# Optimization experiments

Measured on AMD Instinct MI355X. Metric: run time of the kernel, lower is better.

Reference implementation:

```python
import jax, jax.numpy as jnp
import numpy as np

H, W = 64, 64

def _fft_mask(h, w):
    # matches torch: W -> W//2+1 for rfft; linspace(-1,1,H) x linspace(0,1,W//2+1)
    wr = w // 2 + 1
    ys = np.linspace(-1.0, 1.0, h)
    xs = np.linspace(0.0, 1.0, wr)
    Y, X = np.meshgrid(ys, xs, indexing='ij')
    return (np.abs(X) < 0.1) | (np.abs(Y) < 0.1) | (X ** 2 + Y ** 2 <= 0.4 ** 2)

_MASK = _fft_mask(H, W)
_IY, _IX = np.nonzero(_MASK)            # static gather indices, K = mask.sum()
_K = int(_MASK.sum())


def setup_inputs() -> dict:
    key = jax.random.key(0)
    k1, k2, k3 = jax.random.split(key, 3)
    S, P, C = 16, 256, 3
    enc_dim = 1024
    mask_dim = 6 * _K                    # real+imag, C=3 channels -> 2*3*K
    x = jax.random.normal(k1, (S, P, C, H, W), dtype=jnp.float32)
    bc_mask = jnp.zeros((H, W), dtype=bool)
    proj_w = jax.random.normal(k2, (enc_dim, mask_dim), dtype=jnp.float32) / np.sqrt(mask_dim)
    proj_b = jax.random.normal(k3, (enc_dim,), dtype=jnp.float32) * 0.01
    return {"x": x, "bc_mask": bc_mask, "proj_w": proj_w, "proj_b": proj_b}


def reference(x, bc_mask, proj_w, proj_b):
    S, P, C = x.shape[0], x.shape[1], x.shape[2]
    fft_x = jnp.fft.rfft2(x)                       # (S,P,C,H,W//2+1) complex
    fft_x = jnp.fft.fftshift(fft_x, axes=-2)       # shift along H
    # boolean-mask gather (row-major over (H, W//2+1) per (s,p,c)), then flatten C*K
    filt = fft_x[..., _IY, _IX]                    # (S,P,C,K)
    filt = filt.reshape(S, P, C * _K)
    feats = jnp.concatenate([jnp.real(filt), jnp.imag(filt)], axis=-1)  # (S,P,6K)
    return feats @ proj_w.T + proj_b               # (S,P,enc_dim)
```

## Files before the change

### kernel.cpp

```cpp
#include <hip/hip_runtime.h>
#include <hip/hip_bf16.h>
#include <math.h>

typedef float f32x4 __attribute__((ext_vector_type(4)));
typedef __bf16 bf16x8 __attribute__((ext_vector_type(8)));

#define PI2 6.283185307179586

static __device__ __forceinline__ unsigned short f2b(float f) {
  __hip_bfloat16 h = __float2bfloat16(f);
  return reinterpret_cast<unsigned short&>(h);
}

__global__ __launch_bounds__(256) void setup_tables_kernel(
    unsigned short* __restrict__ post16, __hip_bfloat16* __restrict__ Tt,
    __hip_bfloat16* __restrict__ Ub) {
  const int tid = threadIdx.x;
  __shared__ int cnt[64];
  __shared__ int pref[64];

  if (tid < 64) {
    int i = tid;
    double ys = -1.0 + (double)i * (2.0 / 63.0);
    int cRow = 0;
    for (int j = 0; j < 33; ++j) {
      double xs = (double)j / 32.0;
      bool m = (fabs(xs) < 0.1) || (fabs(ys) < 0.1) || (xs * xs + ys * ys <= 0.16);
      cRow += m ? 1 : 0;
    }
    cnt[i] = cRow;
  }
  __syncthreads();
  if (tid == 0) {
    int s = 0;
    for (int i = 0; i < 64; ++i) { pref[i] = s; s += cnt[i]; }
  }
  __syncthreads();
  if (tid < 64) {
    int i = tid;
    int k = pref[i];
    double ys = -1.0 + (double)i * (2.0 / 63.0);
    for (int j = 0; j < 36; ++j) {
      unsigned short v = 0xFFFFu;
      if (j < 33) {
        double xs = (double)j / 32.0;
        bool m = (fabs(xs) < 0.1) || (fabs(ys) < 0.1) || (xs * xs + ys * ys <= 0.16);
        if (m) v = (unsigned short)(k++);
      }
      post16[i * 36 + j] = v;
    }
  }

  for (int idx = tid; idx < 80 * 64; idx += 256) {
    int n = idx >> 6, w = idx & 63;
    float v = 0.0f;
    if (n < 33) {
      int r = (n * w) & 63;
      v = cosf((float)(PI2 / 64.0) * (float)r);
    } else if (n >= 40 && n < 73) {
      int r = ((n - 40) * w) & 63;
      v = -sinf((float)(PI2 / 64.0) * (float)r);
    }
    Tt[idx] = __float2bfloat16(v);
  }

  for (int idx = tid; idx < 128 * 128; idx += 256) {
    int up = idx >> 7, kk = idx & 127;
    int u = up & 63;
    int vfreq = (u + 32) & 63;
    int h = kk & 63;
    int r = (vfreq * h) & 63;
    float cv, sv;
    __sincosf((float)(PI2 / 64.0) * (float)r, &sv, &cv);
    float val;
    if (up < 64) val = (kk < 64) ? cv : sv;
    else         val = (kk < 64) ? -sv : cv;
    Ub[idx] = __float2bfloat16(val);
  }
}

__global__ __launch_bounds__(256) void wconv_kernel(
    const float* __restrict__ W, __hip_bfloat16* __restrict__ wB,
    int N, int Kd, int Kp) {
  int total = N * Kp;
  for (int idx = blockIdx.x * 256 + threadIdx.x; idx < total; idx += gridDim.x * 256) {
    int e = idx / Kp;
    int f = idx - e * Kp;
    float v = (f < Kd) ? W[(size_t)e * Kd + f] : 0.0f;
    wB[idx] = __float2bfloat16(v);
  }
}

#define IMGB 10880
#define POSTB 4608

__global__ __launch_bounds__(256, 4) void fft_mfma_kernel(
    const float* __restrict__ x,
    const __hip_bfloat16* __restrict__ Tt,
    const __hip_bfloat16* __restrict__ Ub,
    const unsigned short* __restrict__ post16,
    __hip_bfloat16* __restrict__ feats,
    int K, int Kp) {
  __shared__ __align__(16) char lds[2 * IMGB + POSTB];
  const int tid = threadIdx.x;
  const int lane = tid & 63;
  const int w = tid >> 6;
  const int wi = w >> 1;
  const int wp = w & 1;
  const int l4 = lane & 15;
  const int q = lane >> 4;
  const int img = blockIdx.x * 2 + wi;
  const int sp = img / 3;
  const int c = img - sp * 3;
  char* ibuf = lds + wi * IMGB;
  unsigned int* fb = (unsigned int*)(ibuf + 8704);
  unsigned short* fbs = (unsigned short*)fb;
  unsigned short* postl = (unsigned short*)(lds + 2 * IMGB);

  const float* xi = x + (size_t)img * 4096;
  float4 st[8];
  #pragma unroll
  for (int r = 0; r < 8; ++r) {
    int row = wp * 32 + r * 4 + q;
    st[r] = *reinterpret_cast<const float4*>(xi + row * 64 + l4 * 4);
  }
  {
    const unsigned int* src = reinterpret_cast<const unsigned int*>(post16);
    unsigned int* dst = reinterpret_cast<unsigned int*>(postl);
    for (int i = tid; i < 1152; i += 256) dst[i] = src[i];
  }
  #pragma unroll
  for (int r = 0; r < 8; ++r) {
    int row = wp * 32 + r * 4 + q;
    int off = row * 128 + (((l4 >> 1) ^ (row & 7)) * 16 + (l4 & 1) * 8);
    ushort4 b;
    b.x = f2b(st[r].x); b.y = f2b(st[r].y); b.z = f2b(st[r].z); b.w = f2b(st[r].w);
    *reinterpret_cast<ushort4*>(ibuf + off) = b;
  }

  f32x4 acc1[2][5] = {};
  #pragma unroll
  for (int ks = 0; ks < 2; ++ks) {
    bf16x8 a1[2], b1[5];
    #pragma unroll
    for (int am = 0; am < 2; ++am) {
      int h = (wp * 2 + am) * 16 + l4;
      int kg = ks * 4 + q;
      a1[am] = *reinterpret_cast<const bf16x8*>(ibuf + h * 128 + ((kg ^ (h & 7)) * 16));
    }
    #pragma unroll
    for (int n = 0; n < 5; ++n) {
      int row = n * 16 + l4;
      b1[n] = *reinterpret_cast<const bf16x8*>(
          (const char*)Tt + row * 128 + ks * 64 + q * 16);
    }
    #pragma unroll
    for (int am = 0; am < 2; ++am)
      #pragma unroll
      for (int n = 0; n < 5; ++n)
        acc1[am][n] = __builtin_amdgcn_mfma_f32_16x16x32_bf16(a1[am], b1[n], acc1[am][n], 0, 0, 0);
  }

  __syncthreads();

  #pragma unroll
  for (int n = 0; n < 5; ++n) {
    int col = n * 16 + l4;
    bool isRe = (col < 33);
    bool isIm = (col >= 40 && col < 73);
    if (!(isRe || isIm)) continue;
    int j = isRe ? col : (col - 40);
    #pragma unroll
    for (int am = 0; am < 2; ++am) {
      #pragma unroll
      for (int r = 0; r < 4; ++r) {
        int h = (wp * 2 + am) * 16 + q * 4 + r;
        int kk = isRe ? h : (h + 64);
        int off = j * 256 + (((kk >> 3) ^ (j & 15)) * 16 + (kk & 7) * 2);
        *reinterpret_cast<unsigned short*>(ibuf + off) = f2b(acc1[am][n][r]);
      }
    }
  }

  __syncthreads();

  f32x4 acc2[3][4] = {};
  #pragma unroll
  for (int ks = 0; ks < 4; ++ks) {
    bf16x8 a2[3], b2[4];
    #pragma unroll
    for (int m = 0; m < 3; ++m) {
      int j = m * 16 + l4;
      if (j > 33) j = 33;
      int kg = ks * 4 + q;
      a2[m] = *reinterpret_cast<const bf16x8*>(ibuf + j * 256 + ((kg ^ (j & 15)) * 16));
    }
    #pragma unroll
    for (int n = 0; n < 4; ++n) {
      int rowg = (wp * 4 + n) * 16 + l4;
      b2[n] = *reinterpret_cast<const bf16x8*>(
          (const char*)Ub + rowg * 256 + ks * 64 + q * 16);
    }
    #pragma unroll
    for (int m = 0; m < 3; ++m)
      #pragma unroll
      for (int n = 0; n < 4; ++n)
        acc2[m][n] = __builtin_amdgcn_mfma_f32_16x16x32_bf16(a2[m], b2[n], acc2[m][n], 0, 0, 0);
  }

  const int base = wp ? K : 0;
  #pragma unroll
  for (int n = 0; n < 4; ++n) {
    int u = n * 16 + l4;
    #pragma unroll
    for (int m = 0; m < 3; ++m) {
      int j0 = m * 16 + q * 4;
      if (j0 > 32) continue;
      ushort4 kv = *reinterpret_cast<const ushort4*>(postl + u * 36 + j0);
      #pragma unroll
      for (int r = 0; r < 4; ++r) {
        int j = j0 + r;
        unsigned short k = (&kv.x)[r];
        if (j < 33 && k != 0xFFFFu)
          fbs[base + k] = f2b(acc2[m][n][r]);
      }
    }
  }

  __syncthreads();

  {
    size_t obase = (size_t)sp * Kp;
    unsigned int* gRe = reinterpret_cast<unsigned int*>(feats + obase + (size_t)c * K);
    unsigned int* gIm = reinterpret_cast<unsigned int*>(feats + obase + (size_t)3 * K + (size_t)c * K);
    const int KD2 = K / 2;
    for (int i = wp * 64 + lane; i < KD2; i += 128) {
      gRe[i] = fb[i];
      gIm[i] = fb[KD2 + i];
    }
    if (wp == 0 && c == 2) {
      unsigned int* gp = reinterpret_cast<unsigned int*>(feats + obase + (size_t)6 * K);
      int padDw = (Kp - 6 * K) / 2;
      if (lane < padDw) gp[lane] = 0u;
    }
  }
}

#define BM 128
#define BN 128
#define BKK 64

__global__ __launch_bounds__(256) void gemm_bias_kernel(
    const __hip_bfloat16* __restrict__ A, const __hip_bfloat16* __restrict__ B,
    const float* __restrict__ bias, float* __restrict__ C,
    int M, int N, int Kp) {
  __shared__ __align__(16) unsigned short As[BM * BKK];
  __shared__ __align__(16) unsigned short Bs[BN * BKK];

  const int tid = threadIdx.x;
  const int lane = tid & 63;
  const int wid = tid >> 6;
  const int wm = wid & 1;
  const int wn = wid >> 1;
  const int nbm = M / BM;
  const int bm = blockIdx.x % nbm;
  const int bn = blockIdx.x / nbm;
  const int row0A = bm * BM;
  const int row0B = bn * BN;

  f32x4 acc[4][4] = {};

  for (int k0 = 0; k0 < Kp; k0 += BKK) {
    #pragma unroll
    for (int i = 0; i < 4; ++i) {
      int qc = i * 256 + tid;
      int r = qc >> 3;
      int cb = (qc & 7) * 16;
      const char* gA = (const char*)A + ((size_t)(row0A + r) * Kp + k0) * 2 + cb;
      const char* gB = (const char*)B + ((size_t)(row0B + r) * Kp + k0) * 2 + cb;
      char* lA = (char*)As + (size_t)(i * 256 + wid * 64) * 16;
      char* lB = (char*)Bs + (size_t)(i * 256 + wid * 64) * 16;
      __builtin_amdgcn_global_load_lds((const __attribute__((address_space(1))) void*)gA,
                                       (__attribute__((address_space(3))) void*)lA, 16, 0, 0);
      __builtin_amdgcn_global_load_lds((const __attribute__((address_space(1))) void*)gB,
                                       (__attribute__((address_space(3))) void*)lB, 16, 0, 0);
    }
    __syncthreads();

    #pragma unroll
    for (int kk = 0; kk < 2; ++kk) {
      bf16x8 afr[4], bfr[4];
      const int ke = kk * 32 + (lane >> 4) * 8;
      #pragma unroll
      for (int m = 0; m < 4; ++m) {
        int rowA = wm * 64 + m * 16 + (lane & 15);
        afr[m] = *reinterpret_cast<const bf16x8*>(&As[rowA * BKK + ke]);
      }
      #pragma unroll
      for (int n = 0; n < 4; ++n) {
        int rowB = wn * 64 + n * 16 + (lane & 15);
        bfr[n] = *reinterpret_cast<const bf16x8*>(&Bs[rowB * BKK + ke]);
      }
      #pragma unroll
      for (int m = 0; m < 4; ++m)
        #pragma unroll
        for (int n = 0; n < 4; ++n)
          acc[m][n] = __builtin_amdgcn_mfma_f32_16x16x32_bf16(afr[m], bfr[n], acc[m][n], 0, 0, 0);
    }
    __syncthreads();
  }

  #pragma unroll
  for (int n = 0; n < 4; ++n) {
    int gcol = row0B + wn * 64 + n * 16 + (lane & 15);
    float bv = bias[gcol];
    #pragma unroll
    for (int m = 0; m < 4; ++m) {
      int grow0 = row0A + wm * 64 + m * 16 + (lane >> 4) * 4;
      #pragma unroll
      for (int r = 0; r < 4; ++r) {
        C[(size_t)(grow0 + r) * N + gcol] = acc[m][n][r] + bv;
      }
    }
  }
}

extern "C" void kernel_launch(void* const* d_in, const int* in_sizes, int n_in,
                              void* d_out, int out_size, void* d_ws, size_t ws_size,
                              hipStream_t stream) {
  const float* x = (const float*)d_in[0];
  const float* W = (const float*)d_in[2];
  const float* bias = (const float*)d_in[3];
  float* out = (float*)d_out;

  const int ENC = in_sizes[3];
  const int Kd = in_sizes[2] / ENC;
  const int K = Kd / 6;
  const int NIMG = in_sizes[0] / 4096;
  const int SP = NIMG / 3;
  const int Kp = (Kd + 63) & ~63;

  char* ws = (char*)d_ws;
  unsigned short* post16 = (unsigned short*)ws;
  __hip_bfloat16* Tt = (__hip_bfloat16*)(ws + 9216);
  __hip_bfloat16* Ub = (__hip_bfloat16*)(ws + 19456);
  __hip_bfloat16* wB = (__hip_bfloat16*)(ws + 52224);
  size_t wBytes = (size_t)ENC * Kp * 2;
  __hip_bfloat16* feats = (__hip_bfloat16*)(ws + 52224 + wBytes);

  setup_tables_kernel<<<1, 256, 0, stream>>>(post16, Tt, Ub);
  wconv_kernel<<<1024, 256, 0, stream>>>(W, wB, ENC, Kd, Kp);
  fft_mfma_kernel<<<NIMG / 2, 256, 0, stream>>>(x, Tt, Ub, post16, feats, K, Kp);
  gemm_bias_kernel<<<(SP / BM) * (ENC / BN), 256, 0, stream>>>(feats, wB, bias, out, SP, ENC, Kp);
}
```

Before: 191.7 us.

## Loop FFT blocks over eight images with register prefetch of next image

Each FFT block now uses two waves instead of four and processes eight images in sequence rather than two in parallel. The post-index table is copied to LDS once per eight images instead of once per two. While the current image's second-stage MFMAs run, the next image's global loads are issued into registers. The stage-1 spectrum write-back now uses vectorized ushort4 stores. In exchange, far fewer waves are launched, so less parallelism is available to hide memory latency, and images within a block are processed serially.

```diff
diff --git a/kernel.cpp b/kernel.cpp
--- a/kernel.cpp
+++ b/kernel.cpp
@@ -91,157 +91,187 @@
   }
 }
 
+#define IMGS 8
 #define IMGB 10880
 #define POSTB 4608
 
-__global__ __launch_bounds__(256, 4) void fft_mfma_kernel(
+__global__ __launch_bounds__(128, 4) void fft_mfma_kernel(
     const float* __restrict__ x,
     const __hip_bfloat16* __restrict__ Tt,
     const __hip_bfloat16* __restrict__ Ub,
     const unsigned short* __restrict__ post16,
     __hip_bfloat16* __restrict__ feats,
     int K, int Kp) {
-  __shared__ __align__(16) char lds[2 * IMGB + POSTB];
+  __shared__ __align__(16) char lds[IMGB + POSTB];
   const int tid = threadIdx.x;
   const int lane = tid & 63;
-  const int w = tid >> 6;
-  const int wi = w >> 1;
-  const int wp = w & 1;
+  const int wp = tid >> 6;
   const int l4 = lane & 15;
   const int q = lane >> 4;
-  const int img = blockIdx.x * 2 + wi;
-  const int sp = img / 3;
-  const int c = img - sp * 3;
-  char* ibuf = lds + wi * IMGB;
-  unsigned int* fb = (unsigned int*)(ibuf + 8704);
+  char* ibuf = lds;
+  unsigned int* fb = (unsigned int*)(lds + 8704);
   unsigned short* fbs = (unsigned short*)fb;
-  unsigned short* postl = (unsigned short*)(lds + 2 * IMGB);
-
-  const float* xi = x + (size_t)img * 4096;
-  float4 st[8];
-  #pragma unroll
-  for (int r = 0; r < 8; ++r) {
-    int row = wp * 32 + r * 4 + q;
-    st[r] = *reinterpret_cast<const float4*>(xi + row * 64 + l4 * 4);
-  }
+  unsigned short* postl = (unsigned short*)(lds + IMGB);
+
+  const int img0 = blockIdx.x * IMGS;
+
   {
     const unsigned int* src = reinterpret_cast<const unsigned int*>(post16);
     unsigned int* dst = reinterpret_cast<unsigned int*>(postl);
-    for (int i = tid; i < 1152; i += 256) dst[i] = src[i];
-  }
-  #pragma unroll
-  for (int r = 0; r < 8; ++r) {
-    int row = wp * 32 + r * 4 + q;
-    int off = row * 128 + (((l4 >> 1) ^ (row & 7)) * 16 + (l4 & 1) * 8);
-    ushort4 b;
-    b.x = f2b(st[r].x); b.y = f2b(st[r].y); b.z = f2b(st[r].z); b.w = f2b(st[r].w);
-    *reinterpret_cast<ushort4*>(ibuf + off) = b;
-  }
-
-  f32x4 acc1[2][5] = {};
-  #pragma unroll
-  for (int ks = 0; ks < 2; ++ks) {
-    bf16x8 a1[2], b1[5];
-    #pragma unroll
-    for (int am = 0; am < 2; ++am) {
-      int h = (wp * 2 + am) * 16 + l4;
-      int kg = ks * 4 + q;
-      a1[am] = *reinterpret_cast<const bf16x8*>(ibuf + h * 128 + ((kg ^ (h & 7)) * 16));
-    }
+    #pragma unroll
+    for (int i = 0; i < 9; ++i) dst[i * 128 + tid] = src[i * 128 + tid];
+  }
+
+  float4 st[8];
+  {
+    const float* xi = x + (size_t)img0 * 4096;
+    #pragma unroll
+    for (int r = 0; r < 8; ++r) {
+      int row = wp * 32 + r * 4 + q;
+      st[r] = *reinterpret_cast<const float4*>(xi + row * 64 + l4 * 4);
+    }
+    #pragma unroll
+    for (int r = 0; r < 8; ++r) {
+      int row = wp * 32 + r * 4 + q;
+      int off = row * 128 + (((l4 >> 1) ^ (row & 7)) * 16 + (l4 & 1) * 8);
+      ushort4 b;
+      b.x = f2b(st[r].x); b.y = f2b(st[r].y); b.z = f2b(st[r].z); b.w = f2b(st[r].w);
+      *reinterpret_cast<ushort4*>(ibuf + off) = b;
+    }
+  }
+
+  for (int it = 0; it < IMGS; ++it) {
+    const int img = img0 + it;
+    const int sp = img / 3;
+    const int c = img - sp * 3;
+
+    f32x4 acc1[2][5] = {};
+    #pragma unroll
+    for (int ks = 0; ks < 2; ++ks) {
+      bf16x8 a1[2], b1[5];
+      #pragma unroll
+      for (int am = 0; am < 2; ++am) {
+        int h = wp * 32 + am * 16 + l4;
+        int kg = ks * 4 + q;
+        a1[am] = *reinterpret_cast<const bf16x8*>(ibuf + h * 128 + ((kg ^ (h & 7)) * 16));
+      }
+      #pragma unroll
+      for (int n = 0; n < 5; ++n) {
+        int row = n * 16 + l4;
+        b1[n] = *reinterpret_cast<const bf16x8*>(
+            (const char*)Tt + row * 128 + ks * 64 + q * 16);
+      }
+      #pragma unroll
+      for (int am = 0; am < 2; ++am)
+        #pragma unroll
+        for (int n = 0; n < 5; ++n)
+          acc1[am][n] = __builtin_amdgcn_mfma_f32_16x16x32_bf16(a1[am], b1[n], acc1[am][n], 0, 0, 0);
+    }
+
+    __syncthreads();
+
     #pragma unroll
     for (int n = 0; n < 5; ++n) {
-      int row = n * 16 + l4;
-      b1[n] = *reinterpret_cast<const bf16x8*>(
-          (const char*)Tt + row * 128 + ks * 64 + q * 16);
-    }
-    #pragma unroll
-    for (int am = 0; am < 2; ++am)
-      #pragma unroll
-      for (int n = 0; n < 5; ++n)
-        acc1[am][n] = __builtin_amdgcn_mfma_f32_16x16x32_bf16(a1[am], b1[n], acc1[am][n], 0, 0, 0);
-  }
-
-  __syncthreads();
-
-  #pragma unroll
-  for (int n = 0; n < 5; ++n) {
-    int col = n * 16 + l4;
-    bool isRe = (col < 33);
-    bool isIm = (col >= 40 && col < 73);
-    if (!(isRe || isIm)) continue;
-    int j = isRe ? col : (col - 40);
-    #pragma unroll
-    for (int am = 0; am < 2; ++am) {
-      #pragma unroll
-      for (int r = 0; r < 4; ++r) {
-        int h = (wp * 2 + am) * 16 + q * 4 + r;
-        int kk = isRe ? h : (h + 64);
-        int off = j * 256 + (((kk >> 3) ^ (j & 15)) * 16 + (kk & 7) * 2);
-        *reinterpret_cast<unsigned short*>(ibuf + off) = f2b(acc1[am][n][r]);
-      }
-    }
-  }
-
-  __syncthreads();
-
-  f32x4 acc2[3][4] = {};
-  #pragma unroll
-  for (int ks = 0; ks < 4; ++ks) {
-    bf16x8 a2[3], b2[4];
-    #pragma unroll
-    for (int m = 0; m < 3; ++m) {
-      int j = m * 16 + l4;
-      if (j > 33) j = 33;
-      int kg = ks * 4 + q;
-      a2[m] = *reinterpret_cast<const bf16x8*>(ibuf + j * 256 + ((kg ^ (j & 15)) * 16));
-    }
-    #pragma unroll
-    for (int n = 0; n < 4; ++n) {
-      int rowg = (wp * 4 + n) * 16 + l4;
-      b2[n] = *reinterpret_cast<const bf16x8*>(
-          (const char*)Ub + rowg * 256 + ks * 64 + q * 16);
-    }
-    #pragma unroll
-    for (int m = 0; m < 3; ++m)
-      #pragma unroll
-      for (int n = 0; n < 4; ++n)
-        acc2[m][n] = __builtin_amdgcn_mfma_f32_16x16x32_bf16(a2[m], b2[n], acc2[m][n], 0, 0, 0);
-  }
-
-  const int base = wp ? K : 0;
-  #pragma unroll
-  for (int n = 0; n < 4; ++n) {
-    int u = n * 16 + l4;
-    #pragma unroll
-    for (int m = 0; m < 3; ++m) {
-      int j0 = m * 16 + q * 4;
-      if (j0 > 32) continue;
-      ushort4 kv = *reinterpret_cast<const ushort4*>(postl + u * 36 + j0);
-      #pragma unroll
-      for (int r = 0; r < 4; ++r) {
-        int j = j0 + r;
-        unsigned short k = (&kv.x)[r];
-        if (j < 33 && k != 0xFFFFu)
-          fbs[base + k] = f2b(acc2[m][n][r]);
-      }
-    }
-  }
-
-  __syncthreads();
-
-  {
-    size_t obase = (size_t)sp * Kp;
-    unsigned int* gRe = reinterpret_cast<unsigned int*>(feats + obase + (size_t)c * K);
-    unsigned int* gIm = reinterpret_cast<unsigned int*>(feats + obase + (size_t)3 * K + (size_t)c * K);
-    const int KD2 = K / 2;
-    for (int i = wp * 64 + lane; i < KD2; i += 128) {
-      gRe[i] = fb[i];
-      gIm[i] = fb[KD2 + i];
-    }
-    if (wp == 0 && c == 2) {
-      unsigned int* gp = reinterpret_cast<unsigned int*>(feats + obase + (size_t)6 * K);
-      int padDw = (Kp - 6 * K) / 2;
-      if (lane < padDw) gp[lane] = 0u;
+      int col = n * 16 + l4;
+      bool isRe = (col < 33);
+      bool isIm = (col >= 40 && col < 73);
+      if (!(isRe || isIm)) continue;
+      int j = isRe ? col : (col - 40);
+      #pragma unroll
+      for (int am = 0; am < 2; ++am) {
+        int h0 = wp * 32 + am * 16 + q * 4;
+        int kk0 = isRe ? h0 : (h0 + 64);
+        int off = j * 256 + (((kk0 >> 3) ^ (j & 15)) * 16 + (kk0 & 7) * 2);
+        ushort4 b;
+        b.x = f2b(acc1[am][n][0]); b.y = f2b(acc1[am][n][1]);
+        b.z = f2b(acc1[am][n][2]); b.w = f2b(acc1[am][n][3]);
+        *reinterpret_cast<ushort4*>(ibuf + off) = b;
+      }
+    }
+
+    if (it + 1 < IMGS) {
+      const float* xn = x + (size_t)(img + 1) * 4096;
+      #pragma unroll
+      for (int r = 0; r < 8; ++r) {
+        int row = wp * 32 + r * 4 + q;
+        st[r] = *reinterpret_cast<const float4*>(xn + row * 64 + l4 * 4);
+      }
+    }
+
+    __syncthreads();
+
+    f32x4 acc2[3][4] = {};
+    #pragma unroll
+    for (int ks = 0; ks < 4; ++ks) {
+      bf16x8 a2[3], b2[4];
+      #pragma unroll
+      for (int m = 0; m < 3; ++m) {
+        int j = m * 16 + l4;
+        if (j > 33) j = 33;
+        int kg = ks * 4 + q;
+        a2[m] = *reinterpret_cast<const bf16x8*>(ibuf + j * 256 + ((kg ^ (j & 15)) * 16));
+      }
+      #pragma unroll
+      for (int n = 0; n < 4; ++n) {
+        int rowg = (wp * 4 + n) * 16 + l4;
+        b2[n] = *reinterpret_cast<const bf16x8*>(
+            (const char*)Ub + rowg * 256 + ks * 64 + q * 16);
+      }
+      #pragma unroll
+      for (int m = 0; m < 3; ++m)
+        #pragma unroll
+        for (int n = 0; n < 4; ++n)
+          acc2[m][n] = __builtin_amdgcn_mfma_f32_16x16x32_bf16(a2[m], b2[n], acc2[m][n], 0, 0, 0);
+    }
+
+    {
+      const int base = wp ? K : 0;
+      #pragma unroll
+      for (int n = 0; n < 4; ++n) {
+        int u = n * 16 + l4;
+        #pragma unroll
+        for (int m = 0; m < 3; ++m) {
+          int j0 = m * 16 + q * 4;
+          if (j0 > 32) continue;
+          ushort4 kv = *reinterpret_cast<const ushort4*>(postl + u * 36 + j0);
+          #pragma unroll
+          for (int r = 0; r < 4; ++r) {
+            int j = j0 + r;
+            unsigned short k = (&kv.x)[r];
+            if (j < 33 && k != 0xFFFFu)
+              fbs[base + k] = f2b(acc2[m][n][r]);
+          }
+        }
+      }
+    }
+
+    __syncthreads();
+
+    {
+      size_t obase = (size_t)sp * Kp;
+      unsigned int* gRe = reinterpret_cast<unsigned int*>(feats + obase + (size_t)c * K);
+      unsigned int* gIm = reinterpret_cast<unsigned int*>(feats + obase + (size_t)3 * K + (size_t)c * K);
+      const int KD2 = K / 2;
+      for (int i = tid; i < KD2; i += 128) {
+        gRe[i] = fb[i];
+        gIm[i] = fb[KD2 + i];
+      }
+      if (wp == 0 && c == 2) {
+        unsigned int* gp = reinterpret_cast<unsigned int*>(feats + obase + (size_t)6 * K);
+        int padDw = (Kp - 6 * K) / 2;
+        if (lane < padDw) gp[lane] = 0u;
+      }
+    }
+
+    if (it + 1 < IMGS) {
+      #pragma unroll
+      for (int r = 0; r < 8; ++r) {
+        int row = wp * 32 + r * 4 + q;
+        int off = row * 128 + (((l4 >> 1) ^ (row & 7)) * 16 + (l4 & 1) * 8);
+        ushort4 b;
+        b.x = f2b(st[r].x); b.y = f2b(st[r].y); b.z = f2b(st[r].z); b.w = f2b(st[r].w);
+        *reinterpret_cast<ushort4*>(ibuf + off) = b;
+      }
     }
   }
 }
@@ -350,6 +380,6 @@
 
   setup_tables_kernel<<<1, 256, 0, stream>>>(post16, Tt, Ub);
   wconv_kernel<<<1024, 256, 0, stream>>>(W, wB, ENC, Kd, Kp);
-  fft_mfma_kernel<<<NIMG / 2, 256, 0, stream>>>(x, Tt, Ub, post16, feats, K, Kp);
+  fft_mfma_kernel<<<NIMG / IMGS, 128, 0, stream>>>(x, Tt, Ub, post16, feats, K, Kp);
   gemm_bias_kernel<<<(SP / BM) * (ENC / BN), 256, 0, stream>>>(feats, wB, bias, out, SP, ENC, Kp);
 }
```

Measured after the change: 342.1 us. 78.4% more time.

## Split FFT into two kernels with LDS-resident twiddle table for second stage

Applied to the files above, without the earlier changes.

The fused per-image FFT kernel becomes two kernels. The first does the row DFT and writes the intermediate bf16 spectrum to a global scratch buffer. The second stages the pre-swizzled column-DFT twiddle matrix into LDS with direct global-to-LDS loads, and each wave then computes a full image's column transform reading twiddles from LDS rather than global memory. The scatter writes are also packed into ushort4 stores. In exchange it adds an extra global round trip of the intermediate (about 8 KB per image), an extra launch, and lower occupancy in the second kernel.

```diff
diff --git a/kernel.cpp b/kernel.cpp
--- a/kernel.cpp
+++ b/kernel.cpp
@@ -75,7 +75,8 @@
     float val;
     if (up < 64) val = (kk < 64) ? cv : sv;
     else         val = (kk < 64) ? -sv : cv;
-    Ub[idx] = __float2bfloat16(val);
+    int off = up * 256 + (((kk >> 3) ^ (up & 15)) * 16) + (kk & 7) * 2;
+    *reinterpret_cast<unsigned short*>((char*)Ub + off) = f2b(val);
   }
 }
 
@@ -91,17 +92,11 @@
   }
 }
 
-#define IMGB 10880
-#define POSTB 4608
-
-__global__ __launch_bounds__(256, 4) void fft_mfma_kernel(
+__global__ __launch_bounds__(256, 4) void s1_kernel(
     const float* __restrict__ x,
     const __hip_bfloat16* __restrict__ Tt,
-    const __hip_bfloat16* __restrict__ Ub,
-    const unsigned short* __restrict__ post16,
-    __hip_bfloat16* __restrict__ feats,
-    int K, int Kp) {
-  __shared__ __align__(16) char lds[2 * IMGB + POSTB];
+    unsigned int* __restrict__ S2) {
+  __shared__ __align__(16) char lds[2 * 8704];
   const int tid = threadIdx.x;
   const int lane = tid & 63;
   const int w = tid >> 6;
@@ -110,32 +105,24 @@
   const int l4 = lane & 15;
   const int q = lane >> 4;
   const int img = blockIdx.x * 2 + wi;
-  const int sp = img / 3;
-  const int c = img - sp * 3;
-  char* ibuf = lds + wi * IMGB;
-  unsigned int* fb = (unsigned int*)(ibuf + 8704);
-  unsigned short* fbs = (unsigned short*)fb;
-  unsigned short* postl = (unsigned short*)(lds + 2 * IMGB);
-
-  const float* xi = x + (size_t)img * 4096;
-  float4 st[8];
-  #pragma unroll
-  for (int r = 0; r < 8; ++r) {
-    int row = wp * 32 + r * 4 + q;
-    st[r] = *reinterpret_cast<const float4*>(xi + row * 64 + l4 * 4);
-  }
+  char* ibuf = lds + wi * 8704;
+
   {
-    const unsigned int* src = reinterpret_cast<const unsigned int*>(post16);
-    unsigned int* dst = reinterpret_cast<unsigned int*>(postl);
-    for (int i = tid; i < 1152; i += 256) dst[i] = src[i];
-  }
-  #pragma unroll
-  for (int r = 0; r < 8; ++r) {
-    int row = wp * 32 + r * 4 + q;
-    int off = row * 128 + (((l4 >> 1) ^ (row & 7)) * 16 + (l4 & 1) * 8);
-    ushort4 b;
-    b.x = f2b(st[r].x); b.y = f2b(st[r].y); b.z = f2b(st[r].z); b.w = f2b(st[r].w);
-    *reinterpret_cast<ushort4*>(ibuf + off) = b;
+    const float* xi = x + (size_t)img * 4096;
+    float4 st[8];
+    #pragma unroll
+    for (int r = 0; r < 8; ++r) {
+      int row = wp * 32 + r * 4 + q;
+      st[r] = *reinterpret_cast<const float4*>(xi + row * 64 + l4 * 4);
+    }
+    #pragma unroll
+    for (int r = 0; r < 8; ++r) {
+      int row = wp * 32 + r * 4 + q;
+      int off = row * 128 + (((l4 >> 1) ^ (row & 7)) * 16 + (l4 & 1) * 8);
+      ushort4 b;
+      b.x = f2b(st[r].x); b.y = f2b(st[r].y); b.z = f2b(st[r].z); b.w = f2b(st[r].w);
+      *reinterpret_cast<ushort4*>(ibuf + off) = b;
+    }
   }
 
   f32x4 acc1[2][5] = {};
@@ -144,7 +131,7 @@
     bf16x8 a1[2], b1[5];
     #pragma unroll
     for (int am = 0; am < 2; ++am) {
-      int h = (wp * 2 + am) * 16 + l4;
+      int h = wp * 32 + am * 16 + l4;
       int kg = ks * 4 + q;
       a1[am] = *reinterpret_cast<const bf16x8*>(ibuf + h * 128 + ((kg ^ (h & 7)) * 16));
     }
@@ -172,73 +159,125 @@
     int j = isRe ? col : (col - 40);
     #pragma unroll
     for (int am = 0; am < 2; ++am) {
+      int h0 = wp * 32 + am * 16 + q * 4;
+      int kk0 = isRe ? h0 : (h0 + 64);
+      int off = j * 256 + (((kk0 >> 3) ^ (j & 15)) * 16 + (kk0 & 7) * 2);
+      ushort4 b;
+      b.x = f2b(acc1[am][n][0]); b.y = f2b(acc1[am][n][1]);
+      b.z = f2b(acc1[am][n][2]); b.w = f2b(acc1[am][n][3]);
+      *reinterpret_cast<ushort4*>(ibuf + off) = b;
+    }
+  }
+
+  __syncthreads();
+
+  {
+    const int t2 = tid & 127;
+    unsigned int* dst = S2 + (size_t)img * 2112;
+    const char* src = ibuf;
+    #pragma unroll
+    for (int ii = 0; ii < 17; ++ii) {
+      int i = ii * 128 + t2;
+      if (i < 2112) {
+        int j = i >> 6, dw = i & 63;
+        unsigned int v = *reinterpret_cast<const unsigned int*>(
+            src + j * 256 + (((dw >> 2) ^ (j & 15)) * 16) + (dw & 3) * 4);
+        dst[j * 64 + dw] = v;
+      }
+    }
+  }
+}
+
+__global__ __launch_bounds__(256, 3) void s2_kernel(
+    const char* __restrict__ S2,
+    const __hip_bfloat16* __restrict__ Ub,
+    const unsigned short* __restrict__ post16,
+    __hip_bfloat16* __restrict__ feats,
+    int K, int Kp) {
+  __shared__ __align__(16) char lds[32768 + 4608 + 4 * 2176];
+  const int tid = threadIdx.x;
+  const int lane = tid & 63;
+  const int w = tid >> 6;
+  const int l4 = lane & 15;
+  const int q = lane >> 4;
+  char* ubl = lds;
+  unsigned short* postl = (unsigned short*)(lds + 32768);
+  unsigned short* fbs = (unsigned short*)(lds + 32768 + 4608 + w * 2176);
+
+  {
+    #pragma unroll
+    for (int i = 0; i < 8; ++i) {
+      const char* g = (const char*)Ub + (size_t)(i * 256 + w * 64 + lane) * 16;
+      char* l = ubl + (size_t)(i * 256 + w * 64) * 16;
+      __builtin_amdgcn_global_load_lds(
+          (const __attribute__((address_space(1))) void*)g,
+          (__attribute__((address_space(3))) void*)l, 16, 0, 0);
+    }
+    const unsigned int* src = reinterpret_cast<const unsigned int*>(post16);
+    unsigned int* dst = reinterpret_cast<unsigned int*>(postl);
+    #pragma unroll
+    for (int i = 0; i < 5; ++i) {
+      int idx = i * 256 + tid;
+      if (idx < 1152) dst[idx] = src[idx];
+    }
+  }
+  asm volatile("s_waitcnt vmcnt(0)" ::: "memory");
+  __syncthreads();
+
+  const int img = blockIdx.x * 4 + w;
+  const int sp = img / 3;
+  const int c = img - sp * 3;
+  const char* Bimg = S2 + (size_t)img * 8448;
+
+  f32x4 acc[8][3] = {};
+  #pragma unroll
+  for (int ks = 0; ks < 4; ++ks) {
+    bf16x8 bfr[3];
+    #pragma unroll
+    for (int n = 0; n < 3; ++n) {
+      bfr[n] = *reinterpret_cast<const bf16x8*>(
+          Bimg + (n * 16 + l4) * 256 + ks * 64 + q * 16);
+    }
+    #pragma unroll
+    for (int m = 0; m < 8; ++m) {
+      int row = m * 16 + l4;
+      bf16x8 afr = *reinterpret_cast<const bf16x8*>(
+          ubl + row * 256 + (((ks * 4 + q) ^ (row & 15)) * 16));
+      #pragma unroll
+      for (int n = 0; n < 3; ++n)
+        acc[m][n] = __builtin_amdgcn_mfma_f32_16x16x32_bf16(afr, bfr[n], acc[m][n], 0, 0, 0);
+    }
+  }
+
+  #pragma unroll
+  for (int n = 0; n < 3; ++n) {
+    int col = n * 16 + l4;
+    if (col > 32) continue;
+    #pragma unroll
+    for (int m = 0; m < 8; ++m) {
       #pragma unroll
       for (int r = 0; r < 4; ++r) {
-        int h = (wp * 2 + am) * 16 + q * 4 + r;
-        int kk = isRe ? h : (h + 64);
-        int off = j * 256 + (((kk >> 3) ^ (j & 15)) * 16 + (kk & 7) * 2);
-        *reinterpret_cast<unsigned short*>(ibuf + off) = f2b(acc1[am][n][r]);
-      }
-    }
-  }
-
-  __syncthreads();
-
-  f32x4 acc2[3][4] = {};
-  #pragma unroll
-  for (int ks = 0; ks < 4; ++ks) {
-    bf16x8 a2[3], b2[4];
-    #pragma unroll
-    for (int m = 0; m < 3; ++m) {
-      int j = m * 16 + l4;
-      if (j > 33) j = 33;
-      int kg = ks * 4 + q;
-      a2[m] = *reinterpret_cast<const bf16x8*>(ibuf + j * 256 + ((kg ^ (j & 15)) * 16));
-    }
-    #pragma unroll
-    for (int n = 0; n < 4; ++n) {
-      int rowg = (wp * 4 + n) * 16 + l4;
-      b2[n] = *reinterpret_cast<const bf16x8*>(
-          (const char*)Ub + rowg * 256 + ks * 64 + q * 16);
-    }
-    #pragma unroll
-    for (int m = 0; m < 3; ++m)
-      #pragma unroll
-      for (int n = 0; n < 4; ++n)
-        acc2[m][n] = __builtin_amdgcn_mfma_f32_16x16x32_bf16(a2[m], b2[n], acc2[m][n], 0, 0, 0);
-  }
-
-  const int base = wp ? K : 0;
-  #pragma unroll
-  for (int n = 0; n < 4; ++n) {
-    int u = n * 16 + l4;
-    #pragma unroll
-    for (int m = 0; m < 3; ++m) {
-      int j0 = m * 16 + q * 4;
-      if (j0 > 32) continue;
-      ushort4 kv = *reinterpret_cast<const ushort4*>(postl + u * 36 + j0);
-      #pragma unroll
-      for (int r = 0; r < 4; ++r) {
-        int j = j0 + r;
-        unsigned short k = (&kv.x)[r];
-        if (j < 33 && k != 0xFFFFu)
-          fbs[base + k] = f2b(acc2[m][n][r]);
-      }
-    }
-  }
-
-  __syncthreads();
+        int row = m * 16 + q * 4 + r;
+        int u = row & 63;
+        int base = (row >> 6) ? K : 0;
+        unsigned short k = postl[u * 36 + col];
+        if (k != 0xFFFFu)
+          fbs[base + k] = f2b(acc[m][n][r]);
+      }
+    }
+  }
 
   {
     size_t obase = (size_t)sp * Kp;
+    const unsigned int* fb = reinterpret_cast<const unsigned int*>(fbs);
     unsigned int* gRe = reinterpret_cast<unsigned int*>(feats + obase + (size_t)c * K);
     unsigned int* gIm = reinterpret_cast<unsigned int*>(feats + obase + (size_t)3 * K + (size_t)c * K);
     const int KD2 = K / 2;
-    for (int i = wp * 64 + lane; i < KD2; i += 128) {
+    for (int i = lane; i < KD2; i += 64) {
       gRe[i] = fb[i];
       gIm[i] = fb[KD2 + i];
     }
-    if (wp == 0 && c == 2) {
+    if (c == 2) {
       unsigned int* gp = reinterpret_cast<unsigned int*>(feats + obase + (size_t)6 * K);
       int padDw = (Kp - 6 * K) / 2;
       if (lane < padDw) gp[lane] = 0u;
@@ -347,9 +386,12 @@
   __hip_bfloat16* wB = (__hip_bfloat16*)(ws + 52224);
   size_t wBytes = (size_t)ENC * Kp * 2;
   __hip_bfloat16* feats = (__hip_bfloat16*)(ws + 52224 + wBytes);
+  size_t featsBytes = (size_t)SP * Kp * 2;
+  char* S2 = ws + 52224 + wBytes + featsBytes;
 
   setup_tables_kernel<<<1, 256, 0, stream>>>(post16, Tt, Ub);
   wconv_kernel<<<1024, 256, 0, stream>>>(W, wB, ENC, Kd, Kp);
-  fft_mfma_kernel<<<NIMG / 2, 256, 0, stream>>>(x, Tt, Ub, post16, feats, K, Kp);
+  s1_kernel<<<NIMG / 2, 256, 0, stream>>>(x, Tt, (unsigned int*)S2);
+  s2_kernel<<<NIMG / 4, 256, 0, stream>>>(S2, Ub, post16, feats, K, Kp);
   gemm_bias_kernel<<<(SP / BM) * (ENC / BN), 256, 0, stream>>>(feats, wB, bias, out, SP, ENC, Kp);
 }
```

Result: slower. 204.8 us (+6.8%).
